# Performance work log

Hardware: AMD Instinct MI355X
Metric: run time of the kernel (lower is better)

## Reference

```python
import jax, jax.numpy as jnp
import numpy as np

INC, OUTC, NHEADS, KSIZE = 256, 256, 8, 5


def setup_inputs() -> dict:
    key = jax.random.key(0)
    k1, k2 = jax.random.split(key, 2)
    x = jax.random.normal(k1, (4, INC, 64, 64), dtype=jnp.float32)
    w_qkv = jax.random.normal(k2, (3 * OUTC, INC), dtype=jnp.float32) * 0.02
    b_qkv = jnp.zeros((3 * OUTC,), dtype=jnp.float32)
    return {"x": x, "w_qkv": w_qkv, "b_qkv": b_qkv}


def reference(x, w_qkv, b_qkv):
    N, Cin, H, W = x.shape
    hd = OUTC // NHEADS
    ofs = KSIZE // 2
    K2 = KSIZE * KSIZE

    # 1x1 conv == pointwise matmul over channels
    qkv = jnp.einsum('nchw,dc->ndhw', x, w_qkv) + b_qkv[None, :, None, None]
    Q = qkv[:, :OUTC]
    K = qkv[:, OUTC:2 * OUTC]
    V = qkv[:, 2 * OUTC:]

    # Zero-pad K/V; track validity so boundary softmax only spans in-bounds
    # positions (the torch code slices smaller windows at borders -> no pad
    # contribution to softmax).
    Kp = jnp.pad(K, ((0, 0), (0, 0), (ofs, ofs), (ofs, ofs)))
    Vp = jnp.pad(V, ((0, 0), (0, 0), (ofs, ofs), (ofs, ofs)))
    valid = jnp.pad(jnp.ones((H, W), dtype=bool), ((ofs, ofs), (ofs, ofs)))

    # Sliding windows via KSIZE^2 static shifted slices: [N,D,H,W,K2]
    k_win = jnp.stack([Kp[:, :, dy:dy + H, dx:dx + W]
                       for dy in range(KSIZE) for dx in range(KSIZE)], axis=-1)
    v_win = jnp.stack([Vp[:, :, dy:dy + H, dx:dx + W]
                       for dy in range(KSIZE) for dx in range(KSIZE)], axis=-1)
    m_win = jnp.stack([valid[dy:dy + H, dx:dx + W]
                       for dy in range(KSIZE) for dx in range(KSIZE)], axis=-1)  # [H,W,K2]

    qh = Q.reshape(N, NHEADS, hd, H, W)
    kh = k_win.reshape(N, NHEADS, hd, H, W, K2)
    vh = v_win.reshape(N, NHEADS, hd, H, W, K2)

    scores = jnp.einsum('ngdhw,ngdhwk->nghwk', qh, kh)          # [N,G,H,W,K2]
    scores = jnp.where(m_win[None, None], scores, -jnp.inf)
    att = jax.nn.softmax(scores, axis=-1)
    out = jnp.einsum('nghwk,ngdhwk->ngdhw', att, vh)            # [N,G,hd,H,W]
    return out.reshape(N, OUTC, H, W)
```

## Files before the change

### kernel.cpp

```cpp
#include <hip/hip_runtime.h>
#include <hip/hip_bf16.h>
#include <math.h>

#define CIN 256
#define COUT 768
#define OUTC 256
#define HH 64
#define WW 64
#define HW 4096

typedef unsigned int uint32;
typedef unsigned short ushort16;
typedef unsigned long long u64;

using short8 = __attribute__((ext_vector_type(8))) short;
using f32x4  = __attribute__((ext_vector_type(4))) float;
using hf2    = __attribute__((ext_vector_type(2))) _Float16;

__device__ inline uint32 pkbf2(float a, float b) {
    __hip_bfloat162 h = __float22bfloat162_rn(make_float2(a, b));
    union { __hip_bfloat162 h2; uint32 u; } cv; cv.h2 = h;
    return cv.u;
}
__device__ inline uint32 pkhf2(float a, float b) {
    union { _Float16 h[2]; uint32 u; } cv;
    cv.h[0] = (_Float16)a; cv.h[1] = (_Float16)b;
    return cv.u;
}
__device__ inline float f16lo(uint32 u) {
    union { uint32 u; _Float16 h[2]; } c; c.u = u; return (float)c.h[0];
}
__device__ inline float f16hi(uint32 u) {
    union { uint32 u; _Float16 h[2]; } c; c.u = u; return (float)c.h[1];
}
__device__ inline float dpp_xor1(float x) {
#if __has_builtin(__builtin_amdgcn_update_dpp)
    int i = __builtin_amdgcn_update_dpp(0, __float_as_int(x),
                                        0xB1, 0xF, 0xF, true);
    return __int_as_float(i);
#else
    return __shfl_xor(x, 1, 64);
#endif
}

__device__ inline float dot2acc(hf2 a, hf2 b, float c) {
#if __has_builtin(__builtin_amdgcn_fdot2)
    return __builtin_amdgcn_fdot2(a, b, c, false);
#else
    c = fmaf((float)a[0], (float)b[0], c);
    return fmaf((float)a[1], (float)b[1], c);
#endif
}

#define LDSTR 40

__global__ __launch_bounds__(256) void qkv_gemm_kernel(
    const float* __restrict__ x, const float* __restrict__ wq,
    const float* __restrict__ bq, ushort16* __restrict__ qkv)
{
    __shared__ __align__(16) char smem[32768];
    ushort16* As = (ushort16*)smem;
    ushort16* Bs = (ushort16*)smem + 128 * LDSTR;

    const int n   = blockIdx.z;
    const int d0  = blockIdx.y * 128;
    const int p0  = blockIdx.x * 128;
    const int tid = threadIdx.x;
    const int lane = tid & 63;
    const int wid  = tid >> 6;
    const int wm = wid >> 1;
    const int wn = wid & 1;

    const float* xb = x + (size_t)n * CIN * HW;

    const int arow = tid >> 2;
    const int akk  = (tid & 3) * 8;
    const float* aptr = wq + (size_t)(d0 + arow) * CIN + akk;
    const int bkg = (tid >> 6) * 8;
    const int bpg = (tid & 63) * 2;
    const float* bptr = xb + (size_t)bkg * HW + p0 + bpg;

    ushort16* awr0 = &As[arow * LDSTR + akk];
    ushort16* awr1 = &As[(arow + 64) * LDSTR + akk];
    ushort16* bwr0 = &Bs[bpg * LDSTR + bkg];
    ushort16* bwr1 = &Bs[(bpg + 1) * LDSTR + bkg];

    f32x4 acc[4][4];
    #pragma unroll
    for (int i = 0; i < 4; ++i)
        #pragma unroll
        for (int j = 0; j < 4; ++j) acc[i][j] = (f32x4){0.f, 0.f, 0.f, 0.f};

    float4 a_st[4];
    float2 b_st[8];

    {
        a_st[0] = *(const float4*)(aptr);
        a_st[1] = *(const float4*)(aptr + 4);
        a_st[2] = *(const float4*)(aptr + (size_t)64 * CIN);
        a_st[3] = *(const float4*)(aptr + (size_t)64 * CIN + 4);
        #pragma unroll
        for (int j = 0; j < 8; ++j)
            b_st[j] = *(const float2*)(bptr + (size_t)j * HW);
    }

    const int lrow = lane & 15;
    const int lk   = (lane >> 4) * 8;

    #pragma unroll 1
    for (int kt = 0; kt < 8; ++kt) {
        __syncthreads();

        {
            uint32 w0 = pkbf2(a_st[0].x, a_st[0].y), w1 = pkbf2(a_st[0].z, a_st[0].w);
            uint32 w2 = pkbf2(a_st[1].x, a_st[1].y), w3 = pkbf2(a_st[1].z, a_st[1].w);
            *(uint4*)awr0 = make_uint4(w0, w1, w2, w3);
            w0 = pkbf2(a_st[2].x, a_st[2].y); w1 = pkbf2(a_st[2].z, a_st[2].w);
            w2 = pkbf2(a_st[3].x, a_st[3].y); w3 = pkbf2(a_st[3].z, a_st[3].w);
            *(uint4*)awr1 = make_uint4(w0, w1, w2, w3);
            uint4 c0, c1;
            c0.x = pkbf2(b_st[0].x, b_st[1].x); c0.y = pkbf2(b_st[2].x, b_st[3].x);
            c0.z = pkbf2(b_st[4].x, b_st[5].x); c0.w = pkbf2(b_st[6].x, b_st[7].x);
            c1.x = pkbf2(b_st[0].y, b_st[1].y); c1.y = pkbf2(b_st[2].y, b_st[3].y);
            c1.z = pkbf2(b_st[4].y, b_st[5].y); c1.w = pkbf2(b_st[6].y, b_st[7].y);
            *(uint4*)bwr0 = c0;
            *(uint4*)bwr1 = c1;
        }

        if (kt < 7) {
            const int ko = (kt + 1) * 32;
            a_st[0] = *(const float4*)(aptr + ko);
            a_st[1] = *(const float4*)(aptr + ko + 4);
            a_st[2] = *(const float4*)(aptr + (size_t)64 * CIN + ko);
            a_st[3] = *(const float4*)(aptr + (size_t)64 * CIN + ko + 4);
            #pragma unroll
            for (int j = 0; j < 8; ++j)
                b_st[j] = *(const float2*)(bptr + (size_t)(ko + j) * HW);
        }

        __syncthreads();

        short8 af[4], bf[4];
        #pragma unroll
        for (int fm = 0; fm < 4; ++fm)
            af[fm] = *(const short8*)&As[(wm * 64 + fm * 16 + lrow) * LDSTR + lk];
        #pragma unroll
        for (int fn = 0; fn < 4; ++fn)
            bf[fn] = *(const short8*)&Bs[(wn * 64 + fn * 16 + lrow) * LDSTR + lk];
        #pragma unroll
        for (int fm = 0; fm < 4; ++fm)
            #pragma unroll
            for (int fn = 0; fn < 4; ++fn)
                acc[fm][fn] = __builtin_amdgcn_mfma_f32_16x16x32_bf16(
                    af[fm], bf[fn], acc[fm][fn], 0, 0, 0);
    }

    __syncthreads();

    u64* E = (u64*)smem + (size_t)wid * 1024;

    const int hi4 = lane >> 4;
    #pragma unroll
    for (int fm = 0; fm < 4; ++fm) {
        const int D = d0 + wm * 64 + fm * 16 + hi4 * 4;
        const float4 bias = *(const float4*)(&bq[D]);
        const int cell = fm * 2 + (hi4 >> 1);
        const int half = hi4 & 1;
        #pragma unroll
        for (int fn = 0; fn < 4; ++fn) {
            const int pl = fn * 16 + lrow;
            f32x4 v = acc[fm][fn];
            u64 pk = (u64)pkhf2(v[0] + bias.x, v[1] + bias.y)
                   | ((u64)pkhf2(v[2] + bias.z, v[3] + bias.w) << 32);
            E[pl * 16 + (cell ^ (pl & 7)) * 2 + half] = pk;
        }
    }
    const int pl4 = lane >> 2;
    const int dq  = lane & 3;
    ushort16* qn = qkv + (size_t)n * COUT * HW;
    #pragma unroll
    for (int s = 0; s < 2; ++s) {
        const int D = d0 + wm * 64 + s * 32;
        const int slot = D >> 5;
        ushort16* sb = qn + (size_t)slot * (HW * 32);
        #pragma unroll
        for (int g = 0; g < 4; ++g) {
            const int prow = g * 16 + pl4;
            const int c = s * 4 + dq;
            const uint4 val = *(const uint4*)&E[prow * 16 + ((c ^ (prow & 7)) * 2)];
            *(uint4*)(sb + (size_t)(p0 + wn * 64 + prow) * 32 + dq * 8) = val;
        }
    }
}

#define TR 4
#define TC 32
#define HR 8
#define HC 36
#define NPIX (HR*HC)

__global__ __launch_bounds__(256) void attn_kernel(
    const ushort16* __restrict__ qkv, float* __restrict__ out)
{
    __shared__ uint4 Ks[NPIX * 4];
    __shared__ uint4 Vs[NPIX * 4];

    const int n    = blockIdx.z;
    const int head = blockIdx.y;
    const int ht = blockIdx.x >> 1;
    const int wt = blockIdx.x & 1;
    const int h0 = ht * TR;
    const int w0 = wt * TC;

    const int tid  = threadIdx.x;
    const int half = tid & 1;
    const int wc   = (tid >> 1) & 31;
    const int tr   = tid >> 6;

    const int h = h0 + tr, w = w0 + wc;
    const int p = h * WW + w;

    const uint4* Kb = (const uint4*)(qkv + ((size_t)(n * 24 + 8 + head)) * HW * 32);
    const uint4* Vb = (const uint4*)(qkv + ((size_t)(n * 24 + 16 + head)) * HW * 32);

    for (int c = tid; c < 2 * NPIX * 4; c += 256) {
        const int b  = (c >= NPIX * 4);
        const int cc = c - b * NPIX * 4;
        const int pix = cc >> 2, i = cc & 3;
        const int hr = pix / HC, cw = pix - hr * HC;
        const int hh = h0 + hr - 2, ww = w0 + cw - 2;
        if (hh >= 0 && hh < HH && ww >= 0 && ww < WW) {
            const int pp = hh * WW + ww;
            const uint4 v = (b ? Vb : Kb)[(size_t)pp * 4 + i];
            const int unit = (pix * 4 + i) ^ (pix & 7);
            (b ? Vs : Ks)[unit] = v;
        }
    }

    hf2 q[8];
    {
        const uint4* Qp = (const uint4*)(qkv + (((size_t)(n * 24 + head)) * HW + p) * 32);
        union { uint4 u; hf2 h[4]; } c0, c1;
        c0.u = Qp[half * 2];
        c1.u = Qp[half * 2 + 1];
        #pragma unroll
        for (int i = 0; i < 4; ++i) { q[i] = c0.h[i]; q[4 + i] = c1.h[i]; }
    }

    __syncthreads();

    float sc[25];
    #pragma unroll
    for (int ky = 0; ky < 5; ++ky) {
        const int hh = h + ky - 2;
        const int hr = tr + ky;
        #pragma unroll
        for (int kx = 0; kx < 5; ++kx) {
            const int ww = w + kx - 2;
            float s;
            if (hh >= 0 && hh < HH && ww >= 0 && ww < WW) {
                const int pix = hr * HC + (wc + kx);
                const int u0 = (pix * 4 + half * 2)     ^ (pix & 7);
                const int u1 = (pix * 4 + half * 2 + 1) ^ (pix & 7);
                union { uint4 u; hf2 h[4]; } a, b;
                a.u = Ks[u0]; b.u = Ks[u1];
                float t = 0.f;
                t = dot2acc(q[0], a.h[0], t);
                t = dot2acc(q[1], a.h[1], t);
                t = dot2acc(q[2], a.h[2], t);
                t = dot2acc(q[3], a.h[3], t);
                t = dot2acc(q[4], b.h[0], t);
                t = dot2acc(q[5], b.h[1], t);
                t = dot2acc(q[6], b.h[2], t);
                t = dot2acc(q[7], b.h[3], t);
                s = t;
            } else {
                s = -1e30f;
            }
            sc[ky * 5 + kx] = s;
        }
    }
    #pragma unroll
    for (int k = 0; k < 25; ++k) {
        float o = dpp_xor1(sc[k]);
        sc[k] = (sc[k] <= -1e29f) ? sc[k] : sc[k] + o;
    }

    float m = sc[0];
    #pragma unroll
    for (int k = 1; k < 25; ++k) m = fmaxf(m, sc[k]);
    float sum = 0.f;
    #pragma unroll
    for (int k = 0; k < 25; ++k) {
        float e = __expf(sc[k] - m);
        sc[k] = e;
        sum += e;
    }
    const float inv = 1.f / sum;

    hf2 acch[8];
    #pragma unroll
    for (int i = 0; i < 8; ++i) acch[i] = (hf2){(_Float16)0.f, (_Float16)0.f};
    #pragma unroll
    for (int ky = 0; ky < 5; ++ky) {
        const int hh = h + ky - 2;
        if (hh < 0 || hh >= HH) continue;
        const int hr = tr + ky;
        #pragma unroll
        for (int kx = 0; kx < 5; ++kx) {
            const int ww = w + kx - 2;
            if (ww < 0 || ww >= WW) continue;
            const _Float16 af = (_Float16)sc[ky * 5 + kx];
            const hf2 ah = (hf2){af, af};
            const int pix = hr * HC + (wc + kx);
            const int u0 = (pix * 4 + half * 2)     ^ (pix & 7);
            const int u1 = (pix * 4 + half * 2 + 1) ^ (pix & 7);
            union { uint4 u; hf2 h[4]; } xv, yv;
            xv.u = Vs[u0]; yv.u = Vs[u1];
            acch[0] += ah * xv.h[0];
            acch[1] += ah * xv.h[1];
            acch[2] += ah * xv.h[2];
            acch[3] += ah * xv.h[3];
            acch[4] += ah * yv.h[0];
            acch[5] += ah * yv.h[1];
            acch[6] += ah * yv.h[2];
            acch[7] += ah * yv.h[3];
        }
    }

    float* Ob = out + ((size_t)(n * 8 + head) * 32 + half * 16) * HW + p;
    #pragma unroll
    for (int i = 0; i < 8; ++i) {
        Ob[(size_t)(2*i)   * HW] = (float)acch[i][0] * inv;
        Ob[(size_t)(2*i+1) * HW] = (float)acch[i][1] * inv;
    }
}

extern "C" void kernel_launch(void* const* d_in, const int* in_sizes, int n_in,
                              void* d_out, int out_size, void* d_ws, size_t ws_size,
                              hipStream_t stream) {
    const float* x  = (const float*)d_in[0];
    const float* wq = (const float*)d_in[1];
    const float* bq = (const float*)d_in[2];
    float* out = (float*)d_out;
    ushort16* qkv = (ushort16*)d_ws;

    dim3 g1(HW / 128, COUT / 128, 4);
    qkv_gemm_kernel<<<g1, 256, 0, stream>>>(x, wq, bq, qkv);

    dim3 g2(32, 8, 4);
    attn_kernel<<<g2, 256, 0, stream>>>(qkv, out);
}
```

Baseline: 41.78 us.

## Drop LDS staging in attention; read K/V from global with four lanes per pixel

```diff
diff --git a/kernel.cpp b/kernel.cpp
--- a/kernel.cpp
+++ b/kernel.cpp
@@ -26,12 +26,6 @@
     union { _Float16 h[2]; uint32 u; } cv;
     cv.h[0] = (_Float16)a; cv.h[1] = (_Float16)b;
     return cv.u;
-}
-__device__ inline float f16lo(uint32 u) {
-    union { uint32 u; _Float16 h[2]; } c; c.u = u; return (float)c.h[0];
-}
-__device__ inline float f16hi(uint32 u) {
-    union { uint32 u; _Float16 h[2]; } c; c.u = u; return (float)c.h[1];
 }
 __device__ inline float dpp_xor1(float x) {
 #if __has_builtin(__builtin_amdgcn_update_dpp)
@@ -42,7 +36,15 @@
     return __shfl_xor(x, 1, 64);
 #endif
 }
-
+__device__ inline float dpp_xor2(float x) {
+#if __has_builtin(__builtin_amdgcn_update_dpp)
+    int i = __builtin_amdgcn_update_dpp(0, __float_as_int(x),
+                                        0x4E, 0xF, 0xF, true);
+    return __int_as_float(i);
+#else
+    return __shfl_xor(x, 2, 64);
+#endif
+}
 __device__ inline float dot2acc(hf2 a, hf2 b, float c) {
 #if __has_builtin(__builtin_amdgcn_fdot2)
     return __builtin_amdgcn_fdot2(a, b, c, false);
@@ -193,97 +195,55 @@
     }
 }
 
-#define TR 4
-#define TC 32
-#define HR 8
-#define HC 36
-#define NPIX (HR*HC)
-
 __global__ __launch_bounds__(256) void attn_kernel(
     const ushort16* __restrict__ qkv, float* __restrict__ out)
 {
-    __shared__ uint4 Ks[NPIX * 4];
-    __shared__ uint4 Vs[NPIX * 4];
-
     const int n    = blockIdx.z;
     const int head = blockIdx.y;
-    const int ht = blockIdx.x >> 1;
-    const int wt = blockIdx.x & 1;
-    const int h0 = ht * TR;
-    const int w0 = wt * TC;
+    const int h0 = (blockIdx.x >> 1) * 2;
+    const int w0 = (blockIdx.x & 1) * 32;
 
     const int tid  = threadIdx.x;
-    const int half = tid & 1;
-    const int wc   = (tid >> 1) & 31;
-    const int tr   = tid >> 6;
-
+    const int quar = tid & 3;
+    const int pid  = tid >> 2;
+    const int tr = pid >> 5, wc = pid & 31;
     const int h = h0 + tr, w = w0 + wc;
     const int p = h * WW + w;
 
+    const uint4* Qb = (const uint4*)(qkv + ((size_t)(n * 24 + head)) * HW * 32);
     const uint4* Kb = (const uint4*)(qkv + ((size_t)(n * 24 + 8 + head)) * HW * 32);
     const uint4* Vb = (const uint4*)(qkv + ((size_t)(n * 24 + 16 + head)) * HW * 32);
 
-    for (int c = tid; c < 2 * NPIX * 4; c += 256) {
-        const int b  = (c >= NPIX * 4);
-        const int cc = c - b * NPIX * 4;
-        const int pix = cc >> 2, i = cc & 3;
-        const int hr = pix / HC, cw = pix - hr * HC;
-        const int hh = h0 + hr - 2, ww = w0 + cw - 2;
-        if (hh >= 0 && hh < HH && ww >= 0 && ww < WW) {
-            const int pp = hh * WW + ww;
-            const uint4 v = (b ? Vb : Kb)[(size_t)pp * 4 + i];
-            const int unit = (pix * 4 + i) ^ (pix & 7);
-            (b ? Vs : Ks)[unit] = v;
-        }
-    }
-
-    hf2 q[8];
+    hf2 q[4];
     {
-        const uint4* Qp = (const uint4*)(qkv + (((size_t)(n * 24 + head)) * HW + p) * 32);
-        union { uint4 u; hf2 h[4]; } c0, c1;
-        c0.u = Qp[half * 2];
-        c1.u = Qp[half * 2 + 1];
-        #pragma unroll
-        for (int i = 0; i < 4; ++i) { q[i] = c0.h[i]; q[4 + i] = c1.h[i]; }
-    }
-
-    __syncthreads();
+        union { uint4 u; hf2 h[4]; } c;
+        c.u = Qb[(size_t)p * 4 + quar];
+        #pragma unroll
+        for (int i = 0; i < 4; ++i) q[i] = c.h[i];
+    }
 
     float sc[25];
     #pragma unroll
     for (int ky = 0; ky < 5; ++ky) {
         const int hh = h + ky - 2;
-        const int hr = tr + ky;
         #pragma unroll
         for (int kx = 0; kx < 5; ++kx) {
             const int ww = w + kx - 2;
-            float s;
-            if (hh >= 0 && hh < HH && ww >= 0 && ww < WW) {
-                const int pix = hr * HC + (wc + kx);
-                const int u0 = (pix * 4 + half * 2)     ^ (pix & 7);
-                const int u1 = (pix * 4 + half * 2 + 1) ^ (pix & 7);
-                union { uint4 u; hf2 h[4]; } a, b;
-                a.u = Ks[u0]; b.u = Ks[u1];
-                float t = 0.f;
+            const bool valid = (hh >= 0 && hh < HH && ww >= 0 && ww < WW);
+            float t = 0.f;
+            if (valid) {
+                const int pp = hh * WW + ww;
+                union { uint4 u; hf2 h[4]; } a;
+                a.u = Kb[(size_t)pp * 4 + quar];
                 t = dot2acc(q[0], a.h[0], t);
                 t = dot2acc(q[1], a.h[1], t);
                 t = dot2acc(q[2], a.h[2], t);
                 t = dot2acc(q[3], a.h[3], t);
-                t = dot2acc(q[4], b.h[0], t);
-                t = dot2acc(q[5], b.h[1], t);
-                t = dot2acc(q[6], b.h[2], t);
-                t = dot2acc(q[7], b.h[3], t);
-                s = t;
-            } else {
-                s = -1e30f;
             }
-            sc[ky * 5 + kx] = s;
-        }
-    }
-    #pragma unroll
-    for (int k = 0; k < 25; ++k) {
-        float o = dpp_xor1(sc[k]);
-        sc[k] = (sc[k] <= -1e29f) ? sc[k] : sc[k] + o;
+            t += dpp_xor1(t);
+            t += dpp_xor2(t);
+            sc[ky * 5 + kx] = valid ? t : -1e30f;
+        }
     }
 
     float m = sc[0];
@@ -298,39 +258,32 @@
     }
     const float inv = 1.f / sum;
 
-    hf2 acch[8];
-    #pragma unroll
-    for (int i = 0; i < 8; ++i) acch[i] = (hf2){(_Float16)0.f, (_Float16)0.f};
+    hf2 acch[4];
+    #pragma unroll
+    for (int i = 0; i < 4; ++i) acch[i] = (hf2){(_Float16)0.f, (_Float16)0.f};
     #pragma unroll
     for (int ky = 0; ky < 5; ++ky) {
         const int hh = h + ky - 2;
         if (hh < 0 || hh >= HH) continue;
-        const int hr = tr + ky;
         #pragma unroll
         for (int kx = 0; kx < 5; ++kx) {
             const int ww = w + kx - 2;
             if (ww < 0 || ww >= WW) continue;
             const _Float16 af = (_Float16)sc[ky * 5 + kx];
             const hf2 ah = (hf2){af, af};
-            const int pix = hr * HC + (wc + kx);
-            const int u0 = (pix * 4 + half * 2)     ^ (pix & 7);
-            const int u1 = (pix * 4 + half * 2 + 1) ^ (pix & 7);
-            union { uint4 u; hf2 h[4]; } xv, yv;
-            xv.u = Vs[u0]; yv.u = Vs[u1];
-            acch[0] += ah * xv.h[0];
-            acch[1] += ah * xv.h[1];
-            acch[2] += ah * xv.h[2];
-            acch[3] += ah * xv.h[3];
-            acch[4] += ah * yv.h[0];
-            acch[5] += ah * yv.h[1];
-            acch[6] += ah * yv.h[2];
-            acch[7] += ah * yv.h[3];
-        }
-    }
-
-    float* Ob = out + ((size_t)(n * 8 + head) * 32 + half * 16) * HW + p;
-    #pragma unroll
-    for (int i = 0; i < 8; ++i) {
+            const int pp = hh * WW + ww;
+            union { uint4 u; hf2 h[4]; } v;
+            v.u = Vb[(size_t)pp * 4 + quar];
+            acch[0] += ah * v.h[0];
+            acch[1] += ah * v.h[1];
+            acch[2] += ah * v.h[2];
+            acch[3] += ah * v.h[3];
+        }
+    }
+
+    float* Ob = out + ((size_t)(n * 8 + head) * 32 + quar * 8) * HW + p;
+    #pragma unroll
+    for (int i = 0; i < 4; ++i) {
         Ob[(size_t)(2*i)   * HW] = (float)acch[i][0] * inv;
         Ob[(size_t)(2*i+1) * HW] = (float)acch[i][1] * inv;
     }
@@ -348,6 +301,6 @@
     dim3 g1(HW / 128, COUT / 128, 4);
     qkv_gemm_kernel<<<g1, 256, 0, stream>>>(x, wq, bq, qkv);
 
-    dim3 g2(32, 8, 4);
+    dim3 g2(64, 8, 4);
     attn_kernel<<<g2, 256, 0, stream>>>(qkv, out);
 }
```

Result: slower. 59.60 us (+42.7%).
